# Kernel optimization log

Measured on AMD Instinct MI355X. Metric: run time of the kernel, lower is better.

Reference implementation:

```python
import jax, jax.numpy as jnp
import numpy as np

SEQ = 4096
BLOCK = 64            # sparse_block_size
BLOCKS = SEQ // BLOCK # 64 block rows/cols
NUM_ORACLES = 32
ORACLE = SEQ // NUM_ORACLES      # 128
LOCAL_BLOCKS = ORACLE // BLOCK   # 2 (sliding-window width in blocks)
PATTERN_ID = 0


def _build_block_mask(pattern_id=PATTERN_ID):
    # Mirrors DKernelPredefinedSparseAttention.__init__ create_mask((i,))
    q_pos = np.arange(BLOCKS)[:, None]
    k_pos = np.arange(BLOCKS)[None, :]
    causal = q_pos >= k_pos
    sliding = (q_pos - k_pos) < LOCAL_BLOCKS
    vert = np.zeros(BLOCKS, dtype=bool)
    real_col = int(pattern_id * ORACLE + 0.5)
    cs = real_col // BLOCK
    ce = (real_col + ORACLE) // BLOCK
    vert[cs:ce] = True
    vert[0:1] = True  # global block 0 always visible
    return causal & (sliding | vert[None, :])


def setup_inputs() -> dict:
    key = jax.random.key(0)
    kq, kk, kv = jax.random.split(key, 3)
    shape = (1, SEQ, 8, 128)  # bshd, matches module's own smoke test layout
    q = jax.random.normal(kq, shape, dtype=jnp.float32)
    k = jax.random.normal(kk, shape, dtype=jnp.float32)
    v = jax.random.normal(kv, shape, dtype=jnp.float32)
    block_mask = jnp.asarray(_build_block_mask())  # [BLOCKS, BLOCKS] bool
    return {"q": q, "k": k, "v": v, "block_mask": block_mask}


def reference(q, k, v, block_mask):
    # Expand block-level mask to token level: [S, S]
    tok_mask = jnp.repeat(jnp.repeat(block_mask, BLOCK, axis=0), BLOCK, axis=1)
    scale = 1.0 / jnp.sqrt(jnp.asarray(q.shape[-1], q.dtype))
    # bshd x bshd -> bhqk scores
    scores = jnp.einsum("bqhd,bkhd->bhqk", q, k) * scale
    neg = jnp.asarray(-1e30, scores.dtype)
    scores = jnp.where(tok_mask[None, None, :, :], scores, neg)
    probs = jax.nn.softmax(scores, axis=-1)
    out = jnp.einsum("bhqk,bkhd->bqhd", probs, v)
    return out
```

## Files before the change

kernel.cpp:

```cpp
#include <hip/hip_runtime.h>
#include <hip/hip_bf16.h>

typedef __bf16 bf16x8 __attribute__((ext_vector_type(8)));
typedef float floatx4 __attribute__((ext_vector_type(4)));

constexpr int SEQ = 4096;
constexpr int NH  = 8;
constexpr int DH  = 128;
constexpr int BLK = 64;
constexpr int QBLOCKS = SEQ / BLK;
constexpr int RS = NH * DH;
constexpr float SCALE = 0.088388347648318447f;

static __device__ __align__(16) __bf16 g_Kb[SEQ * NH * DH];
static __device__ __align__(16) __bf16 g_Vt[SEQ * NH * DH];

__device__ __forceinline__ bf16x8 load8f(const float* p) {
    float4 a = *(const float4*)p;
    float4 b = *(const float4*)(p + 4);
    bf16x8 r = { (__bf16)a.x, (__bf16)a.y, (__bf16)a.z, (__bf16)a.w,
                 (__bf16)b.x, (__bf16)b.y, (__bf16)b.z, (__bf16)b.w };
    return r;
}

constexpr int KCELLS = SEQ * NH * DH / 8;

__global__ __launch_bounds__(512) void prepass_kernel(
    const float* __restrict__ K, const float* __restrict__ V)
{
    const int idx = blockIdx.x * 512 + threadIdx.x;
    if (idx < KCELLS) {
        *(bf16x8*)&g_Kb[(size_t)idx * 8] = load8f(K + (size_t)idx * 8);
    } else {
        int c = idx - KCELLS;
        const int lane = c & 63;  c >>= 6;
        const int nt   = c & 7;   c >>= 3;
        const int s2   = c & 1;   c >>= 1;
        const int h    = c & 7;
        const int kb   = c >> 3;
        const int quad = lane >> 4, l16 = lane & 15;
        const float* src = V + (size_t)(kb * BLK + s2 * 32 + quad * 8) * RS
                             + h * DH + nt * 16 + l16;
        bf16x8 r;
#pragma unroll
        for (int j = 0; j < 8; ++j) r[j] = (__bf16)src[(size_t)j * RS];
        *(bf16x8*)&g_Vt[(size_t)(idx - KCELLS) * 8] = r;
    }
}

__global__ __launch_bounds__(512, 4) void sparse_attn_kernel(
    const float* __restrict__ Q,
    float* __restrict__ Out)
{
    const int qb    = blockIdx.x;
    const int h     = blockIdx.y;
    const int tid   = threadIdx.x;
    const int wave  = tid >> 6;
    const int lane  = tid & 63;
    const int strip = wave & 3;
    const int grp   = wave >> 2;
    const int quad  = lane >> 4;
    const int l16   = lane & 15;

    __shared__ __align__(16) __bf16 p_lds[8][16][64];
    __shared__ __align__(16) float  mrg[4 * 16 * 132 + 128];

    constexpr int OSTRIDE = 132;
    constexpr int OSZ     = 16 * OSTRIDE;
    constexpr int MBASE   = 4 * OSZ;
    constexpr int LBASE   = MBASE + 64;

    int blist[4];
    int nb = 0;
    {
        int cand[4] = {0, 1, qb - 1, qb};
        for (int i = 0; i < 4; ++i) {
            int b = cand[i];
            if (b < 0 || b > qb) continue;
            bool dup = false;
            for (int j = 0; j < nb; ++j) dup = dup || (blist[j] == b);
            if (!dup) blist[nb++] = b;
        }
    }

    const bool v0 = (grp < nb);
    const bool v1 = (grp + 2 < nb);
    const int kb0 = v0 ? blist[grp] : 0;
    const int kb1 = v1 ? blist[grp + 2] : 0;

    const int qrow = qb * BLK + strip * 16 + l16;
    const float* qp = Q + (size_t)qrow * RS + h * DH;
    bf16x8 qfrag[4];
#pragma unroll
    for (int s = 0; s < 4; ++s)
        qfrag[s] = load8f(qp + s * 32 + quad * 8);

    floatx4 sfrag[8];
    __builtin_amdgcn_s_setprio(1);
#pragma unroll
    for (int t = 0; t < 2; ++t) {
        const bool valid = t ? v1 : v0;
        const int  kb    = t ? kb1 : kb0;
        if (valid) {
#pragma unroll
            for (int n = 0; n < 4; ++n) {
                floatx4 c = floatx4{0.f, 0.f, 0.f, 0.f};
                const __bf16* kp =
                    g_Kb + (size_t)(kb * BLK + n * 16 + l16) * RS + h * DH;
#pragma unroll
                for (int s = 0; s < 4; ++s) {
                    bf16x8 kf = *(const bf16x8*)(kp + s * 32 + quad * 8);
                    c = __builtin_amdgcn_mfma_f32_16x16x32_bf16(qfrag[s], kf, c, 0, 0, 0);
                }
                sfrag[t * 4 + n] = c;
            }
        } else {
#pragma unroll
            for (int n = 0; n < 4; ++n)
                sfrag[t * 4 + n] = floatx4{-1e30f, -1e30f, -1e30f, -1e30f};
        }
    }
    __builtin_amdgcn_s_setprio(0);

    float m4[4], l4[4];
#pragma unroll
    for (int r = 0; r < 4; ++r) { m4[r] = -1e30f; l4[r] = 0.f; }

    if (v0) {
#pragma unroll
        for (int r = 0; r < 4; ++r) {
            float mx = -1e30f;
#pragma unroll
            for (int i = 0; i < 8; ++i) {
                sfrag[i][r] *= SCALE;
                mx = fmaxf(mx, sfrag[i][r]);
            }
#pragma unroll
            for (int off = 1; off < 16; off <<= 1)
                mx = fmaxf(mx, __shfl_xor(mx, off, 64));
            m4[r] = mx;
        }
#pragma unroll
        for (int r = 0; r < 4; ++r) {
            float rs = 0.f;
#pragma unroll
            for (int i = 0; i < 8; ++i) {
                float p = __expf(sfrag[i][r] - m4[r]);
                sfrag[i][r] = p;
                rs += p;
            }
#pragma unroll
            for (int off = 1; off < 16; off <<= 1)
                rs += __shfl_xor(rs, off, 64);
            l4[r] = rs;
        }
    }

    floatx4 o_acc[8];
#pragma unroll
    for (int n = 0; n < 8; ++n) o_acc[n] = floatx4{0.f, 0.f, 0.f, 0.f};

#pragma unroll
    for (int t = 0; t < 2; ++t) {
        const bool valid = t ? v1 : v0;
        if (!valid) continue;
        const int kb = t ? kb1 : kb0;
        const __bf16* vt = g_Vt + (size_t)(kb * NH + h) * 8192;
#pragma unroll
        for (int n = 0; n < 4; ++n)
#pragma unroll
            for (int r = 0; r < 4; ++r) {
                const int prow = quad * 4 + r;
                const int col  = n * 16 + l16;
                const int idx  = (((col >> 3) ^ (prow & 7)) << 3) | (col & 7);
                p_lds[wave][prow][idx] = (__bf16)sfrag[t * 4 + n][r];
            }
        __builtin_amdgcn_s_setprio(1);
#pragma unroll
        for (int s2 = 0; s2 < 2; ++s2) {
            bf16x8 pa = *(const bf16x8*)
                &p_lds[wave][l16][(((s2 * 4 + quad) ^ (l16 & 7)) << 3)];
#pragma unroll
            for (int n = 0; n < 8; ++n) {
                bf16x8 vb = *(const bf16x8*)
                    (vt + (size_t)((s2 * 8 + n) * 64 + lane) * 8);
                o_acc[n] = __builtin_amdgcn_mfma_f32_16x16x32_bf16(pa, vb, o_acc[n], 0, 0, 0);
            }
        }
        __builtin_amdgcn_s_setprio(0);
    }

    if (grp == 1) {
#pragma unroll
        for (int r = 0; r < 4; ++r) {
            if (l16 == 0) {
                mrg[MBASE + strip * 16 + quad * 4 + r] = m4[r];
                mrg[LBASE + strip * 16 + quad * 4 + r] = l4[r];
            }
#pragma unroll
            for (int n = 0; n < 8; ++n)
                mrg[strip * OSZ + (quad * 4 + r) * OSTRIDE + n * 16 + l16] =
                    o_acc[n][r];
        }
    }

    __syncthreads();

    if (grp == 0) {
        const int orow_base = qb * BLK + strip * 16 + quad * 4;
#pragma unroll
        for (int r = 0; r < 4; ++r) {
            const float m1 = mrg[MBASE + strip * 16 + quad * 4 + r];
            const float l1 = mrg[LBASE + strip * 16 + quad * 4 + r];
            const float M  = fmaxf(m4[r], m1);
            const float a0 = __expf(m4[r] - M);
            const float a1 = __expf(m1 - M);
            const float inv = 1.f / (a0 * l4[r] + a1 * l1);
            float* op = Out + (size_t)(orow_base + r) * RS + h * DH + l16;
#pragma unroll
            for (int n = 0; n < 8; ++n) {
                const float o1 =
                    mrg[strip * OSZ + (quad * 4 + r) * OSTRIDE + n * 16 + l16];
                op[n * 16] = (a0 * o_acc[n][r] + a1 * o1) * inv;
            }
        }
    }
}

extern "C" void kernel_launch(void* const* d_in, const int* in_sizes, int n_in,
                              void* d_out, int out_size, void* d_ws, size_t ws_size,
                              hipStream_t stream) {
    const float* Q = (const float*)d_in[0];
    const float* K = (const float*)d_in[1];
    const float* V = (const float*)d_in[2];
    float* Out = (float*)d_out;

    dim3 pgrid(2 * KCELLS / 512);
    prepass_kernel<<<pgrid, dim3(512), 0, stream>>>(K, V);

    dim3 grid(QBLOCKS, NH);
    sparse_attn_kernel<<<grid, dim3(512), 0, stream>>>(Q, Out);
}
```

Before: 122.4 us.

## Transpose V through LDS in prepass and split attention blocks into halves

The prepass now uses one workgroup per (key block, head). V rows are staged with coalesced float4 loads into padded shared memory and transposed from there, instead of doing strided per-element global reads. The attention kernel splits each query block across two 256-thread workgroups, doubling the grid and halving the LDS per workgroup to raise occupancy and parallelism. The softmax scale is folded into the Q conversion to drop a multiply per score, which changes bf16 rounding slightly.

```diff
diff --git a/kernel.cpp b/kernel.cpp
--- a/kernel.cpp
+++ b/kernel.cpp
@@ -23,52 +23,80 @@
     return r;
 }
 
-constexpr int KCELLS = SEQ * NH * DH / 8;
-
-__global__ __launch_bounds__(512) void prepass_kernel(
+__device__ __forceinline__ bf16x8 load8f_scaled(const float* p, float s) {
+    float4 a = *(const float4*)p;
+    float4 b = *(const float4*)(p + 4);
+    bf16x8 r = { (__bf16)(a.x * s), (__bf16)(a.y * s),
+                 (__bf16)(a.z * s), (__bf16)(a.w * s),
+                 (__bf16)(b.x * s), (__bf16)(b.y * s),
+                 (__bf16)(b.z * s), (__bf16)(b.w * s) };
+    return r;
+}
+
+__global__ __launch_bounds__(256) void prepass_kernel(
     const float* __restrict__ K, const float* __restrict__ V)
 {
-    const int idx = blockIdx.x * 512 + threadIdx.x;
-    if (idx < KCELLS) {
-        *(bf16x8*)&g_Kb[(size_t)idx * 8] = load8f(K + (size_t)idx * 8);
-    } else {
-        int c = idx - KCELLS;
-        const int lane = c & 63;  c >>= 6;
-        const int nt   = c & 7;   c >>= 3;
-        const int s2   = c & 1;   c >>= 1;
-        const int h    = c & 7;
-        const int kb   = c >> 3;
+    __shared__ float vt[64 * 131];
+    const int wg = blockIdx.x;
+    const int t  = threadIdx.x;
+    const int kb = wg >> 3, h = wg & 7;
+
+#pragma unroll
+    for (int i = 0; i < 4; ++i) {
+        const size_t cell = (size_t)wg * 1024 + i * 256 + t;
+        *(bf16x8*)&g_Kb[cell * 8] = load8f(K + cell * 8);
+    }
+
+    const float* vsrc = V + (size_t)(kb * BLK) * RS + h * DH;
+#pragma unroll
+    for (int i = 0; i < 8; ++i) {
+        const int li  = i * 256 + t;
+        const int row = li >> 5;
+        const int c4  = li & 31;
+        const float4 d = *(const float4*)(vsrc + (size_t)row * RS + c4 * 4);
+        float* dst = &vt[row * 131 + c4 * 4];
+        dst[0] = d.x; dst[1] = d.y; dst[2] = d.z; dst[3] = d.w;
+    }
+    __syncthreads();
+
+#pragma unroll
+    for (int i = 0; i < 4; ++i) {
+        const int c    = i * 256 + t;
+        const int lane = c & 63, nt = (c >> 6) & 7, s2 = c >> 9;
         const int quad = lane >> 4, l16 = lane & 15;
-        const float* src = V + (size_t)(kb * BLK + s2 * 32 + quad * 8) * RS
-                             + h * DH + nt * 16 + l16;
+        const int tokb = s2 * 32 + quad * 8;
+        const int d0   = nt * 16 + l16;
         bf16x8 r;
 #pragma unroll
-        for (int j = 0; j < 8; ++j) r[j] = (__bf16)src[(size_t)j * RS];
-        *(bf16x8*)&g_Vt[(size_t)(idx - KCELLS) * 8] = r;
-    }
-}
-
-__global__ __launch_bounds__(512, 4) void sparse_attn_kernel(
+        for (int j = 0; j < 8; ++j)
+            r[j] = (__bf16)vt[(tokb + j) * 131 + d0];
+        *(bf16x8*)&g_Vt[((size_t)wg * 1024 + c) * 8] = r;
+    }
+}
+
+__global__ __launch_bounds__(256, 4) void sparse_attn_kernel(
     const float* __restrict__ Q,
     float* __restrict__ Out)
 {
-    const int qb    = blockIdx.x;
+    const int qb    = blockIdx.x >> 1;
+    const int sub   = blockIdx.x & 1;
     const int h     = blockIdx.y;
     const int tid   = threadIdx.x;
     const int wave  = tid >> 6;
     const int lane  = tid & 63;
-    const int strip = wave & 3;
-    const int grp   = wave >> 2;
+    const int sl    = wave & 1;
+    const int strip = sub * 2 + sl;
+    const int grp   = wave >> 1;
     const int quad  = lane >> 4;
     const int l16   = lane & 15;
 
-    __shared__ __align__(16) __bf16 p_lds[8][16][64];
-    __shared__ __align__(16) float  mrg[4 * 16 * 132 + 128];
+    __shared__ __align__(16) __bf16 p_lds[4][16][64];
+    __shared__ __align__(16) float  mrg[2 * 16 * 132 + 64];
 
     constexpr int OSTRIDE = 132;
     constexpr int OSZ     = 16 * OSTRIDE;
-    constexpr int MBASE   = 4 * OSZ;
-    constexpr int LBASE   = MBASE + 64;
+    constexpr int MBASE   = 2 * OSZ;
+    constexpr int LBASE   = MBASE + 32;
 
     int blist[4];
     int nb = 0;
@@ -93,7 +121,7 @@
     bf16x8 qfrag[4];
 #pragma unroll
     for (int s = 0; s < 4; ++s)
-        qfrag[s] = load8f(qp + s * 32 + quad * 8);
+        qfrag[s] = load8f_scaled(qp + s * 32 + quad * 8, SCALE);
 
     floatx4 sfrag[8];
     __builtin_amdgcn_s_setprio(1);
@@ -131,10 +159,8 @@
         for (int r = 0; r < 4; ++r) {
             float mx = -1e30f;
 #pragma unroll
-            for (int i = 0; i < 8; ++i) {
-                sfrag[i][r] *= SCALE;
+            for (int i = 0; i < 8; ++i)
                 mx = fmaxf(mx, sfrag[i][r]);
-            }
 #pragma unroll
             for (int off = 1; off < 16; off <<= 1)
                 mx = fmaxf(mx, __shfl_xor(mx, off, 64));
@@ -194,12 +220,12 @@
 #pragma unroll
         for (int r = 0; r < 4; ++r) {
             if (l16 == 0) {
-                mrg[MBASE + strip * 16 + quad * 4 + r] = m4[r];
-                mrg[LBASE + strip * 16 + quad * 4 + r] = l4[r];
+                mrg[MBASE + sl * 16 + quad * 4 + r] = m4[r];
+                mrg[LBASE + sl * 16 + quad * 4 + r] = l4[r];
             }
 #pragma unroll
             for (int n = 0; n < 8; ++n)
-                mrg[strip * OSZ + (quad * 4 + r) * OSTRIDE + n * 16 + l16] =
+                mrg[sl * OSZ + (quad * 4 + r) * OSTRIDE + n * 16 + l16] =
                     o_acc[n][r];
         }
     }
@@ -210,8 +236,8 @@
         const int orow_base = qb * BLK + strip * 16 + quad * 4;
 #pragma unroll
         for (int r = 0; r < 4; ++r) {
-            const float m1 = mrg[MBASE + strip * 16 + quad * 4 + r];
-            const float l1 = mrg[LBASE + strip * 16 + quad * 4 + r];
+            const float m1 = mrg[MBASE + sl * 16 + quad * 4 + r];
+            const float l1 = mrg[LBASE + sl * 16 + quad * 4 + r];
             const float M  = fmaxf(m4[r], m1);
             const float a0 = __expf(m4[r] - M);
             const float a1 = __expf(m1 - M);
@@ -220,7 +246,7 @@
 #pragma unroll
             for (int n = 0; n < 8; ++n) {
                 const float o1 =
-                    mrg[strip * OSZ + (quad * 4 + r) * OSTRIDE + n * 16 + l16];
+                    mrg[sl * OSZ + (quad * 4 + r) * OSTRIDE + n * 16 + l16];
                 op[n * 16] = (a0 * o_acc[n][r] + a1 * o1) * inv;
             }
         }
@@ -235,9 +261,8 @@
     const float* V = (const float*)d_in[2];
     float* Out = (float*)d_out;
 
-    dim3 pgrid(2 * KCELLS / 512);
-    prepass_kernel<<<pgrid, dim3(512), 0, stream>>>(K, V);
-
-    dim3 grid(QBLOCKS, NH);
-    sparse_attn_kernel<<<grid, dim3(512), 0, stream>>>(Q, Out);
-}
+    prepass_kernel<<<dim3(QBLOCKS * NH), dim3(256), 0, stream>>>(K, V);
+
+    dim3 grid(QBLOCKS * 2, NH);
+    sparse_attn_kernel<<<grid, dim3(256), 0, stream>>>(Q, Out);
+}
```

Measured after the change: 123.8 us. Within noise of the previous version (+1.2%).
